# Kernel tuning notes

Measured on AMD Instinct MI355X. Metric: run time of the kernel, lower is better.

Reference implementation:

```python
import jax, jax.numpy as jnp
import numpy as np

THRESH = 0.5
MARGIN = 0.1
SCALE_POS = 2.0
SCALE_NEG = 40.0
EPSILON = 1e-5


def setup_inputs() -> dict:
    key = jax.random.key(0)
    kx, kl = jax.random.split(key)
    B, D, N_CLASSES = 4096, 1024, 256
    x = jax.random.normal(kx, (B, D), dtype=jnp.float32)
    # L2-normalize embeddings (standard for multi-similarity loss; keeps sim in [-1, 1])
    x = x / jnp.linalg.norm(x, axis=1, keepdims=True)
    labels = jax.random.randint(kl, (B,), 0, N_CLASSES, dtype=jnp.int64)
    return {"x": x, "labels": labels}


def reference(x, labels):
    B = x.shape[0]
    sim = jnp.matmul(x, x.T)  # [B, B]

    eye = jnp.eye(B, dtype=bool)
    same = labels[:, None] == labels[None, :]
    pos_mask = same & ~eye                      # positives excl. self
    neg_mask = ~same                            # negatives
    pos_valid = pos_mask & (sim < 1.0 - EPSILON)  # pos_pair_ after < 1-eps filter

    # per-row hardest stats (inf/-inf where empty)
    min_pos = jnp.min(jnp.where(pos_valid, sim, jnp.inf), axis=1)   # min over pos_pair_
    max_neg = jnp.max(jnp.where(neg_mask, sim, -jnp.inf), axis=1)   # max over neg_pair_

    # mined pairs
    neg_keep = neg_mask & (sim + MARGIN > min_pos[:, None])
    pos_keep = pos_valid & (sim - MARGIN < max_neg[:, None])

    has_row = (pos_valid.any(axis=1) & neg_mask.any(axis=1)
               & pos_keep.any(axis=1) & neg_keep.any(axis=1))

    pos_sum = jnp.sum(jnp.where(pos_keep, jnp.exp(-SCALE_POS * (sim - THRESH)), 0.0), axis=1)
    neg_sum = jnp.sum(jnp.where(neg_keep, jnp.exp(SCALE_NEG * (sim - THRESH)), 0.0), axis=1)

    pos_loss = jnp.log1p(pos_sum) / SCALE_POS
    neg_loss = jnp.log1p(neg_sum) / SCALE_NEG

    row_loss = jnp.where(has_row, pos_loss + neg_loss, 0.0)
    return jnp.sum(row_loss) / B
```

## Files before the change

kernel.cpp:

```cpp
#include <hip/hip_runtime.h>
#include <hip/hip_bf16.h>
#include <hip/hip_cooperative_groups.h>
#include <math.h>
#include <stdint.h>

namespace cg = cooperative_groups;


#define THRESH    0.5f
#define MARGIN    0.1f
#define SCALE_POS 2.0f
#define SCALE_NEG 40.0f
#define POS_CAP   (1.0f - 1e-5f)

typedef __bf16 bf16x8 __attribute__((ext_vector_type(8)));
typedef float  f32x4  __attribute__((ext_vector_type(4)));

__device__ __forceinline__ uint16_t f2bf(float f) {
  union { float f; uint32_t u; } v; v.f = f;
  uint32_t u = v.u;
  u += 0x7FFFu + ((u >> 16) & 1u);
  return (uint16_t)(u >> 16);
}

__global__ __launch_bounds__(256) void cvt_bf16_kernel(
    const float* __restrict__ x, uint16_t* __restrict__ y, int n) {
  int i = (blockIdx.x * 256 + threadIdx.x) * 4;
  if (i + 3 < n) {
    float4 v = *(const float4*)(x + i);
    ushort4 o;
    o.x = f2bf(v.x); o.y = f2bf(v.y); o.z = f2bf(v.z); o.w = f2bf(v.w);
    *(ushort4*)(y + i) = o;
  }
}

__device__ __forceinline__ unsigned fkey(float f) {
  unsigned u = __float_as_uint(f);
  return (u & 0x80000000u) ? ~u : (u | 0x80000000u);
}
__device__ __forceinline__ float funkey(unsigned k) {
  unsigned u = (k & 0x80000000u) ? (k & 0x7FFFFFFFu) : ~k;
  return __uint_as_float(u);
}

#if defined(__has_builtin)
#if __has_builtin(__builtin_amdgcn_global_load_lds)
#define HAVE_GLL 1
#endif
#endif

__device__ __forceinline__ void stage16(const uint16_t* g, uint16_t* lds_wave_base, int lane) {
#ifdef HAVE_GLL
  __builtin_amdgcn_global_load_lds(
      (const __attribute__((address_space(1))) void*)g,
      (__attribute__((address_space(3))) void*)lds_wave_base, 16, 0, 0);
#else
  *(uint4*)(lds_wave_base + lane * 8) = *(const uint4*)g;
#endif
}

__global__ __launch_bounds__(256, 3) void fused_kernel(
    const uint16_t* __restrict__ X, const int* __restrict__ labels,
    unsigned* __restrict__ minKey, unsigned* __restrict__ maxKey,
    float* __restrict__ psum, float* __restrict__ nsum,
    int B, int D, int NT) {
  __shared__ __align__(16) uint16_t sA[128 * 32];
  __shared__ __align__(16) uint16_t sB[128 * 32];
  __shared__ int rowLab[128], colLab[128];
  __shared__ float rMinp[128], rMaxn[128], cMinp[128], cMaxn[128];

  int rem = blockIdx.x;
  int bi = 0;
  while (rem >= NT - bi) { rem -= NT - bi; ++bi; }
  const int bj = bi + rem;
  const bool diag = (bi == bj);

  const int tid  = threadIdx.x;
  const int wave = tid >> 6;
  const int lane = tid & 63;
  const int waveM = wave >> 1, waveN = wave & 1;
  const int bm = bi * 128;
  const int bn = bj * 128;

  if (tid < 128) rowLab[tid] = labels[bm + tid];
  else           colLab[tid - 128] = labels[bn + tid - 128];

  const int r0 = tid >> 2,         c0 = (tid & 3) * 8;
  const int r1 = (tid + 256) >> 2, c1 = (tid & 3) * 8;

  const uint16_t* gA = X + (size_t)bm * D;
  const uint16_t* gB = X + (size_t)bn * D;

  uint16_t* lA0 = sA + wave * 512;
  uint16_t* lA1 = sA + 2048 + wave * 512;
  uint16_t* lB0 = sB + wave * 512;
  uint16_t* lB1 = sB + 2048 + wave * 512;

  const int fr = lane & 15;
  const int fq = lane >> 4;
  const int aoff = (waveM * 64 + fr) * 32 + fq * 8;
  const int boff = (waveN * 64 + fr) * 32 + fq * 8;

  const uint16_t* sBsrc = diag ? sA : sB;

  f32x4 acc[4][4] = {};

  for (int k0 = 0; k0 < D; k0 += 32) {
    stage16(gA + (size_t)r0 * D + k0 + c0, lA0, lane);
    stage16(gA + (size_t)r1 * D + k0 + c1, lA1, lane);
    if (!diag) {
      stage16(gB + (size_t)r0 * D + k0 + c0, lB0, lane);
      stage16(gB + (size_t)r1 * D + k0 + c1, lB1, lane);
    }
    __syncthreads();

    bf16x8 af[4], bfv[4];
#pragma unroll
    for (int t = 0; t < 4; ++t) af[t]  = *(const bf16x8*)(sA + aoff + t * 512);
#pragma unroll
    for (int t = 0; t < 4; ++t) bfv[t] = *(const bf16x8*)(sBsrc + boff + t * 512);

#pragma unroll
    for (int mt = 0; mt < 4; ++mt)
#pragma unroll
      for (int nt = 0; nt < 4; ++nt)
        acc[mt][nt] = __builtin_amdgcn_mfma_f32_16x16x32_bf16(
            af[mt], bfv[nt], acc[mt][nt], 0, 0, 0);
    __syncthreads();
  }

  int labC[4];
#pragma unroll
  for (int nt = 0; nt < 4; ++nt) labC[nt] = colLab[waveN * 64 + nt * 16 + fr];

  {
    float cMin[4], cMax[4];
#pragma unroll
    for (int nt = 0; nt < 4; ++nt) { cMin[nt] = 1e30f; cMax[nt] = -1e30f; }

#pragma unroll
    for (int mt = 0; mt < 4; ++mt) {
      float rMin[4], rMax[4]; int labR[4];
#pragma unroll
      for (int r = 0; r < 4; ++r) {
        labR[r] = rowLab[waveM * 64 + mt * 16 + fq * 4 + r];
        rMin[r] = 1e30f; rMax[r] = -1e30f;
      }
#pragma unroll
      for (int nt = 0; nt < 4; ++nt) {
        const int cl = waveN * 64 + nt * 16 + fr;
#pragma unroll
        for (int r = 0; r < 4; ++r) {
          const int rl = waveM * 64 + mt * 16 + fq * 4 + r;
          const float s = acc[mt][nt][r];
          if (labR[r] == labC[nt]) {
            if (!(diag && rl == cl) && s < POS_CAP) {
              rMin[r] = fminf(rMin[r], s);
              cMin[nt] = fminf(cMin[nt], s);
            }
          } else {
            rMax[r] = fmaxf(rMax[r], s);
            cMax[nt] = fmaxf(cMax[nt], s);
          }
        }
      }
#pragma unroll
      for (int m = 1; m < 16; m <<= 1)
#pragma unroll
        for (int r = 0; r < 4; ++r) {
          rMin[r] = fminf(rMin[r], __shfl_xor(rMin[r], m, 64));
          rMax[r] = fmaxf(rMax[r], __shfl_xor(rMax[r], m, 64));
        }
      if (fr == 0) {
#pragma unroll
        for (int r = 0; r < 4; ++r) {
          const int row = bm + waveM * 64 + mt * 16 + fq * 4 + r;
          if (rMin[r] < 2.f)  atomicMin(&minKey[row], fkey(rMin[r]));
          if (rMax[r] > -2.f) atomicMax(&maxKey[row], fkey(rMax[r]));
        }
      }
    }

    if (!diag) {
#pragma unroll
      for (int m = 16; m < 64; m <<= 1)
#pragma unroll
        for (int nt = 0; nt < 4; ++nt) {
          cMin[nt] = fminf(cMin[nt], __shfl_xor(cMin[nt], m, 64));
          cMax[nt] = fmaxf(cMax[nt], __shfl_xor(cMax[nt], m, 64));
        }
      if (lane < 16) {
#pragma unroll
        for (int nt = 0; nt < 4; ++nt) {
          const int col = bn + waveN * 64 + nt * 16 + fr;
          if (cMin[nt] < 2.f)  atomicMin(&minKey[col], fkey(cMin[nt]));
          if (cMax[nt] > -2.f) atomicMax(&maxKey[col], fkey(cMax[nt]));
        }
      }
    }
  }

  cg::this_grid().sync();

  if (tid < 128) {
    rMinp[tid] = funkey(minKey[bm + tid]);
    rMaxn[tid] = funkey(maxKey[bm + tid]);
  } else {
    cMinp[tid - 128] = funkey(minKey[bn + tid - 128]);
    cMaxn[tid - 128] = funkey(maxKey[bn + tid - 128]);
  }
  __syncthreads();

  float pCol[4] = {0.f, 0.f, 0.f, 0.f}, nCol[4] = {0.f, 0.f, 0.f, 0.f};

#pragma unroll
  for (int mt = 0; mt < 4; ++mt) {
    float pRow[4] = {0.f, 0.f, 0.f, 0.f}, nRow[4] = {0.f, 0.f, 0.f, 0.f};
    int labR[4]; float rmn[4], rmp[4];
#pragma unroll
    for (int r = 0; r < 4; ++r) {
      const int rl = waveM * 64 + mt * 16 + fq * 4 + r;
      labR[r] = rowLab[rl]; rmn[r] = rMaxn[rl]; rmp[r] = rMinp[rl];
    }
#pragma unroll
    for (int nt = 0; nt < 4; ++nt) {
      const int cl = waveN * 64 + nt * 16 + fr;
      const float cmn = cMaxn[cl], cmp = cMinp[cl];
#pragma unroll
      for (int r = 0; r < 4; ++r) {
        const int rl = waveM * 64 + mt * 16 + fq * 4 + r;
        const float s = acc[mt][nt][r];
        if (labR[r] == labC[nt]) {
          if (!(diag && rl == cl) && s < POS_CAP) {
            const float e = __expf(-SCALE_POS * (s - THRESH));
            if (s - MARGIN < rmn[r]) pRow[r] += e;
            if (s - MARGIN < cmn)    pCol[nt] += e;
          }
        } else {
          const float e = __expf(SCALE_NEG * (s - THRESH));
          if (s + MARGIN > rmp[r]) nRow[r] += e;
          if (s + MARGIN > cmp)    nCol[nt] += e;
        }
      }
    }
#pragma unroll
    for (int m = 1; m < 16; m <<= 1)
#pragma unroll
      for (int r = 0; r < 4; ++r) {
        pRow[r] += __shfl_xor(pRow[r], m, 64);
        nRow[r] += __shfl_xor(nRow[r], m, 64);
      }
    if (fr == 0) {
#pragma unroll
      for (int r = 0; r < 4; ++r) {
        const int row = bm + waveM * 64 + mt * 16 + fq * 4 + r;
        if (pRow[r] != 0.f) atomicAdd(&psum[row], pRow[r]);
        if (nRow[r] != 0.f) atomicAdd(&nsum[row], nRow[r]);
      }
    }
  }

  if (!diag) {
#pragma unroll
    for (int m = 16; m < 64; m <<= 1)
#pragma unroll
      for (int nt = 0; nt < 4; ++nt) {
        pCol[nt] += __shfl_xor(pCol[nt], m, 64);
        nCol[nt] += __shfl_xor(nCol[nt], m, 64);
      }
    if (lane < 16) {
#pragma unroll
      for (int nt = 0; nt < 4; ++nt) {
        const int col = bn + waveN * 64 + nt * 16 + fr;
        if (pCol[nt] != 0.f) atomicAdd(&psum[col], pCol[nt]);
        if (nCol[nt] != 0.f) atomicAdd(&nsum[col], nCol[nt]);
      }
    }
  }
}

__global__ __launch_bounds__(256) void simgemm_mine_kernel(
    const uint16_t* __restrict__ X, const int* __restrict__ labels,
    float* __restrict__ C, unsigned* __restrict__ minKey,
    unsigned* __restrict__ maxKey, int B, int D, int NT) {
  __shared__ __align__(16) uint16_t sA[128 * 32];
  __shared__ __align__(16) uint16_t sB[128 * 32];
  __shared__ int rowLab[128];
  __shared__ int colLab[128];

  int rem = blockIdx.x;
  int bi = 0;
  while (rem >= NT - bi) { rem -= NT - bi; ++bi; }
  const int bj = bi + rem;
  const bool diag = (bi == bj);

  const int tid  = threadIdx.x;
  const int wave = tid >> 6;
  const int lane = tid & 63;
  const int waveM = wave >> 1, waveN = wave & 1;
  const int bm = bi * 128;
  const int bn = bj * 128;

  if (tid < 128) rowLab[tid] = labels[bm + tid];
  else           colLab[tid - 128] = labels[bn + tid - 128];

  const int r0 = tid >> 2,         c0 = (tid & 3) * 8;
  const int r1 = (tid + 256) >> 2, c1 = (tid & 3) * 8;

  const uint16_t* gA = X + (size_t)bm * D;
  const uint16_t* gB = X + (size_t)bn * D;

  uint16_t* lA0 = sA + wave * 512;
  uint16_t* lA1 = sA + 2048 + wave * 512;
  uint16_t* lB0 = sB + wave * 512;
  uint16_t* lB1 = sB + 2048 + wave * 512;

  const int fr = lane & 15;
  const int fq = lane >> 4;
  const int aoff = (waveM * 64 + fr) * 32 + fq * 8;
  const int boff = (waveN * 64 + fr) * 32 + fq * 8;

  const uint16_t* sBsrc = diag ? sA : sB;

  f32x4 acc[4][4] = {};

  for (int k0 = 0; k0 < D; k0 += 32) {
    stage16(gA + (size_t)r0 * D + k0 + c0, lA0, lane);
    stage16(gA + (size_t)r1 * D + k0 + c1, lA1, lane);
    if (!diag) {
      stage16(gB + (size_t)r0 * D + k0 + c0, lB0, lane);
      stage16(gB + (size_t)r1 * D + k0 + c1, lB1, lane);
    }
    __syncthreads();

    bf16x8 af[4], bfv[4];
#pragma unroll
    for (int t = 0; t < 4; ++t) af[t]  = *(const bf16x8*)(sA + aoff + t * 512);
#pragma unroll
    for (int t = 0; t < 4; ++t) bfv[t] = *(const bf16x8*)(sBsrc + boff + t * 512);

#pragma unroll
    for (int mt = 0; mt < 4; ++mt)
#pragma unroll
      for (int nt = 0; nt < 4; ++nt)
        acc[mt][nt] = __builtin_amdgcn_mfma_f32_16x16x32_bf16(
            af[mt], bfv[nt], acc[mt][nt], 0, 0, 0);
    __syncthreads();
  }

#pragma unroll
  for (int mt = 0; mt < 4; ++mt)
#pragma unroll
    for (int nt = 0; nt < 4; ++nt) {
      const int col = bn + waveN * 64 + nt * 16 + fr;
#pragma unroll
      for (int r = 0; r < 4; ++r) {
        const int row = bm + waveM * 64 + mt * 16 + fq * 4 + r;
        C[(size_t)row * B + col] = acc[mt][nt][r];
      }
    }

  int labC[4]; float cMin[4], cMax[4];
#pragma unroll
  for (int nt = 0; nt < 4; ++nt) {
    labC[nt] = colLab[waveN * 64 + nt * 16 + fr];
    cMin[nt] = 1e30f; cMax[nt] = -1e30f;
  }

#pragma unroll
  for (int mt = 0; mt < 4; ++mt) {
    float rMin[4], rMax[4]; int labR[4];
#pragma unroll
    for (int r = 0; r < 4; ++r) {
      labR[r] = rowLab[waveM * 64 + mt * 16 + fq * 4 + r];
      rMin[r] = 1e30f; rMax[r] = -1e30f;
    }
#pragma unroll
    for (int nt = 0; nt < 4; ++nt) {
      const int cl = waveN * 64 + nt * 16 + fr;
#pragma unroll
      for (int r = 0; r < 4; ++r) {
        const int rl = waveM * 64 + mt * 16 + fq * 4 + r;
        const float s = acc[mt][nt][r];
        if (labR[r] == labC[nt]) {
          if (!(diag && rl == cl) && s < POS_CAP) {
            rMin[r] = fminf(rMin[r], s);
            cMin[nt] = fminf(cMin[nt], s);
          }
        } else {
          rMax[r] = fmaxf(rMax[r], s);
          cMax[nt] = fmaxf(cMax[nt], s);
        }
      }
    }
#pragma unroll
    for (int m = 1; m < 16; m <<= 1)
#pragma unroll
      for (int r = 0; r < 4; ++r) {
        rMin[r] = fminf(rMin[r], __shfl_xor(rMin[r], m, 64));
        rMax[r] = fmaxf(rMax[r], __shfl_xor(rMax[r], m, 64));
      }
    if (fr == 0) {
#pragma unroll
      for (int r = 0; r < 4; ++r) {
        const int row = bm + waveM * 64 + mt * 16 + fq * 4 + r;
        if (rMin[r] < 2.f)  atomicMin(&minKey[row], fkey(rMin[r]));
        if (rMax[r] > -2.f) atomicMax(&maxKey[row], fkey(rMax[r]));
      }
    }
  }

  if (!diag) {
#pragma unroll
    for (int m = 16; m < 64; m <<= 1)
#pragma unroll
      for (int nt = 0; nt < 4; ++nt) {
        cMin[nt] = fminf(cMin[nt], __shfl_xor(cMin[nt], m, 64));
        cMax[nt] = fmaxf(cMax[nt], __shfl_xor(cMax[nt], m, 64));
      }
    if (lane < 16) {
#pragma unroll
      for (int nt = 0; nt < 4; ++nt) {
        const int col = bn + waveN * 64 + nt * 16 + fr;
        if (cMin[nt] < 2.f)  atomicMin(&minKey[col], fkey(cMin[nt]));
        if (cMax[nt] > -2.f) atomicMax(&maxKey[col], fkey(cMax[nt]));
      }
    }
  }
}

__global__ __launch_bounds__(256) void exploss_kernel(
    const float* __restrict__ C, const int* __restrict__ labels,
    const unsigned* __restrict__ minKey, const unsigned* __restrict__ maxKey,
    float* __restrict__ psum, float* __restrict__ nsum, int B, int NT) {
  __shared__ int   rLab[32];
  __shared__ float rMinp[32], rMaxn[32];
  __shared__ int   cLab[128];
  __shared__ float cMinp[128], cMaxn[128];
  __shared__ float pCarr[128], nCarr[128];

  int rem = blockIdx.x >> 2;
  const int split = blockIdx.x & 3;
  int bi = 0;
  while (rem >= NT - bi) { rem -= NT - bi; ++bi; }
  const int bj = bi + rem;
  const bool diag = (bi == bj);
  const int bm = bi * 128, bn = bj * 128;
  const int rbase = split * 32;

  const int tid = threadIdx.x;
  if (tid < 32) {
    const int row = bm + rbase + tid;
    rLab[tid]  = labels[row];
    rMinp[tid] = funkey(minKey[row]);
    rMaxn[tid] = funkey(maxKey[row]);
  } else if (tid < 160) {
    const int col = bn + (tid - 32);
    cLab[tid - 32]  = labels[col];
    cMinp[tid - 32] = funkey(minKey[col]);
    cMaxn[tid - 32] = funkey(maxKey[col]);
  }
  if (tid < 128) { pCarr[tid] = 0.f; nCarr[tid] = 0.f; }
  __syncthreads();

  const int rowg = tid >> 5;
  const int c0   = (tid & 31) * 4;
  int labC[4]; float mpC[4], mnC[4];
#pragma unroll
  for (int q = 0; q < 4; ++q) {
    labC[q] = cLab[c0 + q]; mpC[q] = cMinp[c0 + q]; mnC[q] = cMaxn[c0 + q];
  }
  float pCa[4] = {0.f, 0.f, 0.f, 0.f}, nCa[4] = {0.f, 0.f, 0.f, 0.f};

  for (int it = 0; it < 4; ++it) {
    const int rr = rowg + it * 8;
    const int rl = rbase + rr;
    const float4 v = *(const float4*)(C + (size_t)(bm + rl) * B + bn + c0);
    const float sq[4] = {v.x, v.y, v.z, v.w};
    const int   lr  = rLab[rr];
    const float rmn = rMaxn[rr];
    const float rmp = rMinp[rr];
    float pR = 0.f, nR = 0.f;
#pragma unroll
    for (int q = 0; q < 4; ++q) {
      const float s = sq[q];
      if (lr == labC[q]) {
        if (!(diag && rl == c0 + q) && s < POS_CAP) {
          const float e = __expf(-SCALE_POS * (s - THRESH));
          if (s - MARGIN < rmn)    pR += e;
          if (s - MARGIN < mnC[q]) pCa[q] += e;
        }
      } else {
        const float e = __expf(SCALE_NEG * (s - THRESH));
        if (s + MARGIN > rmp)    nR += e;
        if (s + MARGIN > mpC[q]) nCa[q] += e;
      }
    }
#pragma unroll
    for (int m = 1; m < 32; m <<= 1) {
      pR += __shfl_xor(pR, m, 64);
      nR += __shfl_xor(nR, m, 64);
    }
    if ((tid & 31) == 0) {
      atomicAdd(&psum[bm + rl], pR);
      atomicAdd(&nsum[bm + rl], nR);
    }
  }

  if (!diag) {
#pragma unroll
    for (int q = 0; q < 4; ++q) {
      atomicAdd(&pCarr[c0 + q], pCa[q]);
      atomicAdd(&nCarr[c0 + q], nCa[q]);
    }
    __syncthreads();
    if (tid < 128) {
      if (pCarr[tid] != 0.f) atomicAdd(&psum[bn + tid], pCarr[tid]);
      if (nCarr[tid] != 0.f) atomicAdd(&nsum[bn + tid], nCarr[tid]);
    }
  }
}

__global__ __launch_bounds__(1024) void final_kernel(
    const unsigned* __restrict__ minKey, const unsigned* __restrict__ maxKey,
    const float* __restrict__ psum, const float* __restrict__ nsum,
    float* __restrict__ out, int B) {
  __shared__ float red[16];
  const int tid = threadIdx.x;
  float acc = 0.f;
  for (int i = tid; i < B; i += 1024) {
    const unsigned mk = minKey[i], xk = maxKey[i];
    const float p = psum[i], n = nsum[i];
    if (mk != 0xFFFFFFFFu && xk != 0u && p > 0.f && n > 0.f)
      acc += log1pf(p) * (1.0f / SCALE_POS) + log1pf(n) * (1.0f / SCALE_NEG);
  }
#pragma unroll
  for (int m = 32; m > 0; m >>= 1) acc += __shfl_xor(acc, m, 64);
  if ((tid & 63) == 0) red[tid >> 6] = acc;
  __syncthreads();
  if (tid == 0) {
    float t = 0.f;
#pragma unroll
    for (int w = 0; w < 16; ++w) t += red[w];
    out[0] = t / (float)B;
  }
}

extern "C" void kernel_launch(void* const* d_in, const int* in_sizes, int n_in,
                              void* d_out, int out_size, void* d_ws, size_t ws_size,
                              hipStream_t stream) {
  const float* x      = (const float*)d_in[0];
  const int*   labels = (const int*)d_in[1];
  float*       out    = (float*)d_out;

  int B = in_sizes[1];
  int D = in_sizes[0] / B;
  int NT = B / 128;
  const int NTILES = NT * (NT + 1) / 2;

  uint16_t* xbf = (uint16_t*)d_ws;
  size_t xbytes = (((size_t)B * D * 2) + 255) & ~(size_t)255;
  unsigned* minKey = (unsigned*)((char*)d_ws + xbytes);
  unsigned* maxKey = minKey + B;
  float* psumA = (float*)(maxKey + B);
  float* nsumA = psumA + B;
  float* sim   = (float*)((char*)d_ws + xbytes + ((size_t)B * 16 + 255 & ~(size_t)255));

  hipMemsetAsync(minKey, 0xFF, (size_t)B * 4, stream);
  hipMemsetAsync(maxKey, 0x00, (size_t)B * 12, stream);

  const int n = B * D;
  cvt_bf16_kernel<<<n / 1024, 256, 0, stream>>>(x, xbf, n);

  int perMP = 0;
  hipOccupancyMaxActiveBlocksPerMultiprocessor(&perMP, fused_kernel, 256, 0);
  int numMP = 0;
  hipDeviceGetAttribute(&numMP, hipDeviceAttributeMultiprocessorCount, 0);
  const bool coop_ok = (perMP > 0 && numMP > 0 && (long)perMP * numMP >= NTILES);

  if (coop_ok) {
    void* args[] = {(void*)&xbf, (void*)&labels, (void*)&minKey, (void*)&maxKey,
                    (void*)&psumA, (void*)&nsumA, (void*)&B, (void*)&D, (void*)&NT};
    hipLaunchCooperativeKernel((void*)fused_kernel, dim3(NTILES), dim3(256),
                               args, 0, stream);
  } else {
    simgemm_mine_kernel<<<NTILES, 256, 0, stream>>>(xbf, labels, sim, minKey, maxKey, B, D, NT);
    exploss_kernel<<<NTILES * 4, 256, 0, stream>>>(sim, labels, minKey, maxKey, psumA, nsumA, B, NT);
  }

  final_kernel<<<1, 1024, 0, stream>>>(minKey, maxKey, psumA, nsumA, out, B);
}
```

Baseline: 151.2 us.

## Split cooperative tiles into 128x64 halves, fold init and final reduce into kernels

```diff
diff --git a/kernel.cpp b/kernel.cpp
--- a/kernel.cpp
+++ b/kernel.cpp
@@ -23,14 +23,25 @@
   return (uint16_t)(u >> 16);
 }
 
-__global__ __launch_bounds__(256) void cvt_bf16_kernel(
-    const float* __restrict__ x, uint16_t* __restrict__ y, int n) {
+__global__ __launch_bounds__(256) void cvt_init_kernel(
+    const float* __restrict__ x, uint16_t* __restrict__ y, int n,
+    unsigned* __restrict__ minKey, unsigned* __restrict__ maxKey,
+    float* __restrict__ psum, float* __restrict__ nsum, int B) {
   int i = (blockIdx.x * 256 + threadIdx.x) * 4;
   if (i + 3 < n) {
     float4 v = *(const float4*)(x + i);
     ushort4 o;
     o.x = f2bf(v.x); o.y = f2bf(v.y); o.z = f2bf(v.z); o.w = f2bf(v.w);
     *(ushort4*)(y + i) = o;
+  }
+  const int nb = (B + 127) / 128;
+  if (blockIdx.x < (unsigned)nb && threadIdx.x < 128) {
+    const int j = blockIdx.x * 128 + threadIdx.x;
+    if (j < B) {
+      minKey[j] = 0xFFFFFFFFu;
+      maxKey[j] = 0u;
+      psum[j] = 0.f; nsum[j] = 0.f;
+    }
   }
 }
 
@@ -59,84 +70,87 @@
 #endif
 }
 
-__global__ __launch_bounds__(256, 3) void fused_kernel(
+__global__ __launch_bounds__(256, 5) void fused_kernel(
     const uint16_t* __restrict__ X, const int* __restrict__ labels,
     unsigned* __restrict__ minKey, unsigned* __restrict__ maxKey,
     float* __restrict__ psum, float* __restrict__ nsum,
-    int B, int D, int NT) {
+    float* __restrict__ out, int B, int D, int NT) {
   __shared__ __align__(16) uint16_t sA[128 * 32];
-  __shared__ __align__(16) uint16_t sB[128 * 32];
-  __shared__ int rowLab[128], colLab[128];
-  __shared__ float rMinp[128], rMaxn[128], cMinp[128], cMaxn[128];
-
-  int rem = blockIdx.x;
-  int bi = 0;
-  while (rem >= NT - bi) { rem -= NT - bi; ++bi; }
-  const int bj = bi + rem;
+  __shared__ __align__(16) uint16_t sB[64 * 32];
+  __shared__ int   rowLab[128], colLab[64];
+  __shared__ float rMinp[128], rMaxn[128], cMinp[64], cMaxn[64];
+  __shared__ float red[8];
+
+  const int h = blockIdx.x;
+  const int offc = NT * (NT - 1);
+  int bi, bj, side;
+  if (h < offc) {
+    const int s = h >> 1; side = h & 1;
+    int rem = s; bi = 0;
+    while (rem >= NT - 1 - bi) { rem -= NT - 1 - bi; ++bi; }
+    bj = bi + 1 + rem;
+  } else {
+    const int d = h - offc; bi = bj = d >> 1; side = d & 1;
+  }
   const bool diag = (bi == bj);
 
   const int tid  = threadIdx.x;
   const int wave = tid >> 6;
   const int lane = tid & 63;
   const int waveM = wave >> 1, waveN = wave & 1;
-  const int bm = bi * 128;
-  const int bn = bj * 128;
-
-  if (tid < 128) rowLab[tid] = labels[bm + tid];
-  else           colLab[tid - 128] = labels[bn + tid - 128];
-
-  const int r0 = tid >> 2,         c0 = (tid & 3) * 8;
-  const int r1 = (tid + 256) >> 2, c1 = (tid & 3) * 8;
+  const int bm  = bi * 128;
+  const int bnc = bj * 128 + side * 64;
+
+  if (tid < 128)      rowLab[tid] = labels[bm + tid];
+  else if (tid < 192) colLab[tid - 128] = labels[bnc + (tid - 128)];
+
+  const int rA0 = tid >> 2,         cA = (tid & 3) * 8;
+  const int rA1 = (tid + 256) >> 2;
+  const int rB0 = tid >> 2;
 
   const uint16_t* gA = X + (size_t)bm * D;
-  const uint16_t* gB = X + (size_t)bn * D;
+  const uint16_t* gB = X + (size_t)bnc * D;
 
   uint16_t* lA0 = sA + wave * 512;
   uint16_t* lA1 = sA + 2048 + wave * 512;
   uint16_t* lB0 = sB + wave * 512;
-  uint16_t* lB1 = sB + 2048 + wave * 512;
 
   const int fr = lane & 15;
   const int fq = lane >> 4;
   const int aoff = (waveM * 64 + fr) * 32 + fq * 8;
-  const int boff = (waveN * 64 + fr) * 32 + fq * 8;
-
-  const uint16_t* sBsrc = diag ? sA : sB;
-
-  f32x4 acc[4][4] = {};
+  const uint16_t* bsrc = diag ? sA : sB;
+  const int boff = diag ? ((side * 64 + waveN * 32 + fr) * 32 + fq * 8)
+                        : ((waveN * 32 + fr) * 32 + fq * 8);
+
+  f32x4 acc[4][2] = {};
 
   for (int k0 = 0; k0 < D; k0 += 32) {
-    stage16(gA + (size_t)r0 * D + k0 + c0, lA0, lane);
-    stage16(gA + (size_t)r1 * D + k0 + c1, lA1, lane);
-    if (!diag) {
-      stage16(gB + (size_t)r0 * D + k0 + c0, lB0, lane);
-      stage16(gB + (size_t)r1 * D + k0 + c1, lB1, lane);
-    }
+    stage16(gA + (size_t)rA0 * D + k0 + cA, lA0, lane);
+    stage16(gA + (size_t)rA1 * D + k0 + cA, lA1, lane);
+    if (!diag) stage16(gB + (size_t)rB0 * D + k0 + cA, lB0, lane);
     __syncthreads();
 
-    bf16x8 af[4], bfv[4];
-#pragma unroll
-    for (int t = 0; t < 4; ++t) af[t]  = *(const bf16x8*)(sA + aoff + t * 512);
-#pragma unroll
-    for (int t = 0; t < 4; ++t) bfv[t] = *(const bf16x8*)(sBsrc + boff + t * 512);
+    bf16x8 af[4], bfv[2];
+#pragma unroll
+    for (int t = 0; t < 4; ++t) af[t] = *(const bf16x8*)(sA + aoff + t * 512);
+#pragma unroll
+    for (int t = 0; t < 2; ++t) bfv[t] = *(const bf16x8*)(bsrc + boff + t * 512);
 
 #pragma unroll
     for (int mt = 0; mt < 4; ++mt)
 #pragma unroll
-      for (int nt = 0; nt < 4; ++nt)
+      for (int nt = 0; nt < 2; ++nt)
         acc[mt][nt] = __builtin_amdgcn_mfma_f32_16x16x32_bf16(
             af[mt], bfv[nt], acc[mt][nt], 0, 0, 0);
     __syncthreads();
   }
 
-  int labC[4];
-#pragma unroll
-  for (int nt = 0; nt < 4; ++nt) labC[nt] = colLab[waveN * 64 + nt * 16 + fr];
+  int labC[2];
+#pragma unroll
+  for (int nt = 0; nt < 2; ++nt) labC[nt] = colLab[waveN * 32 + nt * 16 + fr];
 
   {
-    float cMin[4], cMax[4];
-#pragma unroll
-    for (int nt = 0; nt < 4; ++nt) { cMin[nt] = 1e30f; cMax[nt] = -1e30f; }
+    float cMin[2] = {1e30f, 1e30f}, cMax[2] = {-1e30f, -1e30f};
 
 #pragma unroll
     for (int mt = 0; mt < 4; ++mt) {
@@ -147,14 +161,14 @@
         rMin[r] = 1e30f; rMax[r] = -1e30f;
       }
 #pragma unroll
-      for (int nt = 0; nt < 4; ++nt) {
-        const int cl = waveN * 64 + nt * 16 + fr;
+      for (int nt = 0; nt < 2; ++nt) {
+        const int cl = waveN * 32 + nt * 16 + fr;
 #pragma unroll
         for (int r = 0; r < 4; ++r) {
           const int rl = waveM * 64 + mt * 16 + fq * 4 + r;
           const float s = acc[mt][nt][r];
           if (labR[r] == labC[nt]) {
-            if (!(diag && rl == cl) && s < POS_CAP) {
+            if (!(diag && rl == side * 64 + cl) && s < POS_CAP) {
               rMin[r] = fminf(rMin[r], s);
               cMin[nt] = fminf(cMin[nt], s);
             }
@@ -185,14 +199,14 @@
 #pragma unroll
       for (int m = 16; m < 64; m <<= 1)
 #pragma unroll
-        for (int nt = 0; nt < 4; ++nt) {
+        for (int nt = 0; nt < 2; ++nt) {
           cMin[nt] = fminf(cMin[nt], __shfl_xor(cMin[nt], m, 64));
           cMax[nt] = fmaxf(cMax[nt], __shfl_xor(cMax[nt], m, 64));
         }
       if (lane < 16) {
 #pragma unroll
-        for (int nt = 0; nt < 4; ++nt) {
-          const int col = bn + waveN * 64 + nt * 16 + fr;
+        for (int nt = 0; nt < 2; ++nt) {
+          const int col = bnc + waveN * 32 + nt * 16 + fr;
           if (cMin[nt] < 2.f)  atomicMin(&minKey[col], fkey(cMin[nt]));
           if (cMax[nt] > -2.f) atomicMax(&maxKey[col], fkey(cMax[nt]));
         }
@@ -205,77 +219,97 @@
   if (tid < 128) {
     rMinp[tid] = funkey(minKey[bm + tid]);
     rMaxn[tid] = funkey(maxKey[bm + tid]);
-  } else {
-    cMinp[tid - 128] = funkey(minKey[bn + tid - 128]);
-    cMaxn[tid - 128] = funkey(maxKey[bn + tid - 128]);
+  } else if (tid < 192) {
+    cMinp[tid - 128] = funkey(minKey[bnc + (tid - 128)]);
+    cMaxn[tid - 128] = funkey(maxKey[bnc + (tid - 128)]);
   }
   __syncthreads();
 
-  float pCol[4] = {0.f, 0.f, 0.f, 0.f}, nCol[4] = {0.f, 0.f, 0.f, 0.f};
-
-#pragma unroll
-  for (int mt = 0; mt < 4; ++mt) {
-    float pRow[4] = {0.f, 0.f, 0.f, 0.f}, nRow[4] = {0.f, 0.f, 0.f, 0.f};
-    int labR[4]; float rmn[4], rmp[4];
-#pragma unroll
-    for (int r = 0; r < 4; ++r) {
-      const int rl = waveM * 64 + mt * 16 + fq * 4 + r;
-      labR[r] = rowLab[rl]; rmn[r] = rMaxn[rl]; rmp[r] = rMinp[rl];
-    }
-#pragma unroll
-    for (int nt = 0; nt < 4; ++nt) {
-      const int cl = waveN * 64 + nt * 16 + fr;
-      const float cmn = cMaxn[cl], cmp = cMinp[cl];
+  {
+    float pCol[2] = {0.f, 0.f}, nCol[2] = {0.f, 0.f};
+
+#pragma unroll
+    for (int mt = 0; mt < 4; ++mt) {
+      float pRow[4] = {0.f, 0.f, 0.f, 0.f}, nRow[4] = {0.f, 0.f, 0.f, 0.f};
+      int labR[4]; float rmn[4], rmp[4];
 #pragma unroll
       for (int r = 0; r < 4; ++r) {
         const int rl = waveM * 64 + mt * 16 + fq * 4 + r;
-        const float s = acc[mt][nt][r];
-        if (labR[r] == labC[nt]) {
-          if (!(diag && rl == cl) && s < POS_CAP) {
-            const float e = __expf(-SCALE_POS * (s - THRESH));
-            if (s - MARGIN < rmn[r]) pRow[r] += e;
-            if (s - MARGIN < cmn)    pCol[nt] += e;
+        labR[r] = rowLab[rl]; rmn[r] = rMaxn[rl]; rmp[r] = rMinp[rl];
+      }
+#pragma unroll
+      for (int nt = 0; nt < 2; ++nt) {
+        const int cl = waveN * 32 + nt * 16 + fr;
+        const float cmn = cMaxn[cl], cmp = cMinp[cl];
+#pragma unroll
+        for (int r = 0; r < 4; ++r) {
+          const int rl = waveM * 64 + mt * 16 + fq * 4 + r;
+          const float s = acc[mt][nt][r];
+          if (labR[r] == labC[nt]) {
+            if (!(diag && rl == side * 64 + cl) && s < POS_CAP) {
+              const float e = __expf(-SCALE_POS * (s - THRESH));
+              if (s - MARGIN < rmn[r]) pRow[r] += e;
+              if (!diag && s - MARGIN < cmn) pCol[nt] += e;
+            }
+          } else {
+            const float e = __expf(SCALE_NEG * (s - THRESH));
+            if (s + MARGIN > rmp[r]) nRow[r] += e;
+            if (!diag && s + MARGIN > cmp) nCol[nt] += e;
           }
-        } else {
-          const float e = __expf(SCALE_NEG * (s - THRESH));
-          if (s + MARGIN > rmp[r]) nRow[r] += e;
-          if (s + MARGIN > cmp)    nCol[nt] += e;
-        }
-      }
-    }
-#pragma unroll
-    for (int m = 1; m < 16; m <<= 1)
-#pragma unroll
-      for (int r = 0; r < 4; ++r) {
-        pRow[r] += __shfl_xor(pRow[r], m, 64);
-        nRow[r] += __shfl_xor(nRow[r], m, 64);
-      }
-    if (fr == 0) {
-#pragma unroll
-      for (int r = 0; r < 4; ++r) {
-        const int row = bm + waveM * 64 + mt * 16 + fq * 4 + r;
-        if (pRow[r] != 0.f) atomicAdd(&psum[row], pRow[r]);
-        if (nRow[r] != 0.f) atomicAdd(&nsum[row], nRow[r]);
-      }
-    }
-  }
-
-  if (!diag) {
-#pragma unroll
-    for (int m = 16; m < 64; m <<= 1)
-#pragma unroll
-      for (int nt = 0; nt < 4; ++nt) {
-        pCol[nt] += __shfl_xor(pCol[nt], m, 64);
-        nCol[nt] += __shfl_xor(nCol[nt], m, 64);
-      }
-    if (lane < 16) {
-#pragma unroll
-      for (int nt = 0; nt < 4; ++nt) {
-        const int col = bn + waveN * 64 + nt * 16 + fr;
-        if (pCol[nt] != 0.f) atomicAdd(&psum[col], pCol[nt]);
-        if (nCol[nt] != 0.f) atomicAdd(&nsum[col], nCol[nt]);
-      }
-    }
+        }
+      }
+#pragma unroll
+      for (int m = 1; m < 16; m <<= 1)
+#pragma unroll
+        for (int r = 0; r < 4; ++r) {
+          pRow[r] += __shfl_xor(pRow[r], m, 64);
+          nRow[r] += __shfl_xor(nRow[r], m, 64);
+        }
+      if (fr == 0) {
+#pragma unroll
+        for (int r = 0; r < 4; ++r) {
+          const int row = bm + waveM * 64 + mt * 16 + fq * 4 + r;
+          if (pRow[r] != 0.f) atomicAdd(&psum[row], pRow[r]);
+          if (nRow[r] != 0.f) atomicAdd(&nsum[row], nRow[r]);
+        }
+      }
+    }
+
+    if (!diag) {
+#pragma unroll
+      for (int m = 16; m < 64; m <<= 1)
+#pragma unroll
+        for (int nt = 0; nt < 2; ++nt) {
+          pCol[nt] += __shfl_xor(pCol[nt], m, 64);
+          nCol[nt] += __shfl_xor(nCol[nt], m, 64);
+        }
+      if (lane < 16) {
+#pragma unroll
+        for (int nt = 0; nt < 2; ++nt) {
+          const int col = bnc + waveN * 32 + nt * 16 + fr;
+          if (pCol[nt] != 0.f) atomicAdd(&psum[col], pCol[nt]);
+          if (nCol[nt] != 0.f) atomicAdd(&nsum[col], nCol[nt]);
+        }
+      }
+    }
+  }
+
+  cg::this_grid().sync();
+
+  if (blockIdx.x == 0) {
+    float accl = 0.f;
+    for (int i = tid; i < B; i += 256) {
+      const unsigned mk = minKey[i], xk = maxKey[i];
+      const float p = psum[i], n = nsum[i];
+      if (mk != 0xFFFFFFFFu && xk != 0u && p > 0.f && n > 0.f)
+        accl += log1pf(p) * (1.0f / SCALE_POS) + log1pf(n) * (1.0f / SCALE_NEG);
+    }
+#pragma unroll
+    for (int m = 32; m > 0; m >>= 1) accl += __shfl_xor(accl, m, 64);
+    if (lane == 0) red[wave] = accl;
+    __syncthreads();
+    if (tid == 0)
+      out[0] = (red[0] + red[1] + red[2] + red[3]) / (float)B;
   }
 }
 
@@ -556,6 +590,7 @@
   int B = in_sizes[1];
   int D = in_sizes[0] / B;
   int NT = B / 128;
+  const int NHALF  = NT * (NT + 1);
   const int NTILES = NT * (NT + 1) / 2;
 
   uint16_t* xbf = (uint16_t*)d_ws;
@@ -564,29 +599,27 @@
   unsigned* maxKey = minKey + B;
   float* psumA = (float*)(maxKey + B);
   float* nsumA = psumA + B;
-  float* sim   = (float*)((char*)d_ws + xbytes + ((size_t)B * 16 + 255 & ~(size_t)255));
-
-  hipMemsetAsync(minKey, 0xFF, (size_t)B * 4, stream);
-  hipMemsetAsync(maxKey, 0x00, (size_t)B * 12, stream);
+  float* sim   = (float*)((char*)d_ws + xbytes + (((size_t)B * 16 + 255) & ~(size_t)255));
 
   const int n = B * D;
-  cvt_bf16_kernel<<<n / 1024, 256, 0, stream>>>(x, xbf, n);
+  cvt_init_kernel<<<n / 1024, 256, 0, stream>>>(x, xbf, n, minKey, maxKey,
+                                                psumA, nsumA, B);
 
   int perMP = 0;
   hipOccupancyMaxActiveBlocksPerMultiprocessor(&perMP, fused_kernel, 256, 0);
   int numMP = 0;
   hipDeviceGetAttribute(&numMP, hipDeviceAttributeMultiprocessorCount, 0);
-  const bool coop_ok = (perMP > 0 && numMP > 0 && (long)perMP * numMP >= NTILES);
+  const bool coop_ok = (perMP > 0 && numMP > 0 && (long)perMP * numMP >= NHALF);
 
   if (coop_ok) {
     void* args[] = {(void*)&xbf, (void*)&labels, (void*)&minKey, (void*)&maxKey,
-                    (void*)&psumA, (void*)&nsumA, (void*)&B, (void*)&D, (void*)&NT};
-    hipLaunchCooperativeKernel((void*)fused_kernel, dim3(NTILES), dim3(256),
+                    (void*)&psumA, (void*)&nsumA, (void*)&out,
+                    (void*)&B, (void*)&D, (void*)&NT};
+    hipLaunchCooperativeKernel((void*)fused_kernel, dim3(NHALF), dim3(256),
                                args, 0, stream);
   } else {
     simgemm_mine_kernel<<<NTILES, 256, 0, stream>>>(xbf, labels, sim, minKey, maxKey, B, D, NT);
     exploss_kernel<<<NTILES * 4, 256, 0, stream>>>(sim, labels, minKey, maxKey, psumA, nsumA, B, NT);
-  }
-
-  final_kernel<<<1, 1024, 0, stream>>>(minKey, maxKey, psumA, nsumA, out, B);
-}
+    final_kernel<<<1, 1024, 0, stream>>>(minKey, maxKey, psumA, nsumA, out, B);
+  }
+}
```

Result: faster. 147.6 us (-2.3%).
